# Kernel optimization log

Measured on AMD Instinct MI355X. Metric: run time of the kernel, lower is better.

Reference implementation:

```python
import jax, jax.numpy as jnp
import numpy as np

B, N, F = 8192, 48, 64      # batch, node_n, features
L = 11                      # stacked GraphConvolution blocks
EPS = 1e-5                  # BatchNorm1d eps


def setup_inputs() -> dict:
    key = jax.random.key(0)
    k0, k1, k2, k3, k4 = jax.random.split(key, 5)
    x = jax.random.normal(k0, (B, N, F), dtype=jnp.float32)
    # xavier-normal-ish GC weights, all layers are F->F (in==out)
    W = jax.random.normal(k1, (L, F, F), dtype=jnp.float32) * np.sqrt(2.0 / (F + F)).astype(np.float32)
    # att init: 0.01 + 0.99 * I  (learned node-mixing matrix)
    att = jnp.tile((0.01 + 0.99 * jnp.eye(N, dtype=jnp.float32))[None], (L, 1, 1))
    bias = 0.02 * jax.random.normal(k2, (L, F), dtype=jnp.float32)
    gamma = 1.0 + 0.1 * jax.random.normal(k3, (L, N * F), dtype=jnp.float32)
    beta = 0.1 * jax.random.normal(k4, (L, N * F), dtype=jnp.float32)
    return {"x": x, "W": W, "att": att, "bias": bias, "gamma": gamma, "beta": beta}


def _gcn_forward(x, W, att, bias, gamma, beta):
    def gc(h, i):
        # support = h @ W[i]; output = att[i] @ support + bias[i]
        support = jnp.einsum('bnf,fg->bng', h, W[i])
        return jnp.einsum('nm,bmg->bng', att[i], support) + bias[i]

    def bn(h, i):
        # BatchNorm1d over flattened (node_n * features), batch statistics
        b = h.shape[0]
        flat = h.reshape(b, -1)
        mu = jnp.mean(flat, axis=0)
        var = jnp.var(flat, axis=0)
        flat = (flat - mu) * jax.lax.rsqrt(var + EPS) * gamma[i] + beta[i]
        return flat.reshape(h.shape)

    def block(h, i):
        return jax.nn.sigmoid(bn(gc(h, i), i))  # dropout p=0 -> identity

    y1 = block(x, 0)
    y2 = block(y1, 1)
    y3 = block(y2, 2)
    y4 = block(y3, 3)
    y5 = block(y4, 4)
    y6 = block(y5, 5)
    y7 = block(y6 + y5, 6)
    y8 = block(y7 + y4, 7)
    y9 = block(y8 + y3, 8)
    y10 = block(y9 + y2, 9)
    y11 = block(y10 + y1, 10)  # in_features == out_features
    return y11 + x


def reference(x, W, att, bias, gamma, beta):
    return _gcn_forward(x, W, att, bias, gamma, beta)
```

## Files before the change

### kernel.cpp

```cpp
#include <hip/hip_runtime.h>

#define NBATCH 8192
#define NFEAT  3072
#define TOT    ((size_t)NBATCH * NFEAT)
#define ZBYTES (TOT * 2)
#define YBYTES (TOT)

typedef unsigned short u16;
typedef unsigned int   u32;
typedef unsigned char  u8;

typedef __attribute__((ext_vector_type(8))) short bf16x8;
typedef __attribute__((ext_vector_type(4))) float f32x4;

__device__ __forceinline__ float sigm(float u) {
  return 1.0f / (1.0f + __expf(-u));
}
__device__ __forceinline__ u16 f2b(float f) {
  const u32 u = __float_as_uint(f);
  return (u16)((u + 0x7FFFu + ((u >> 16) & 1u)) >> 16);
}
__device__ __forceinline__ float b2f(u16 h) {
  return __uint_as_float(((u32)h) << 16);
}
__device__ __forceinline__ u32 pack2(float a, float b) {
  return (u32)f2b(a) | ((u32)f2b(b) << 16);
}

template <int MODE>
__global__ __launch_bounds__(256, 2)
void gcn_layer(const void* in0v,
               const u8*  yres_in,
               u8*        yres_out,
               u16*       zout,
               const float* __restrict__ Wg,
               const float* __restrict__ Ag,
               const float* __restrict__ biasg,
               const float* __restrict__ gam0,
               const float* __restrict__ bet0,
               const float* __restrict__ sum0,
               const float* __restrict__ sq0,
               float* __restrict__ osum,
               float* __restrict__ osq)
{
  __shared__ __align__(16) char HlB[2][6144];
  __shared__ __align__(16) char STB[8192];

  const int t    = threadIdx.x;
  const int lane = t & 63;
  const int wv   = t >> 6;
  const int lr   = lane & 15;
  const int lk   = lane >> 4;

  bf16x8 Wf[2];
  #pragma unroll
  for (int ks = 0; ks < 2; ++ks)
    #pragma unroll
    for (int j = 0; j < 8; ++j) {
      const int k = ks * 32 + lk * 8 + j;
      Wf[ks][j] = (short)f2b(Wg[k * 64 + wv * 16 + lr]);
    }
  bf16x8 Af[3][2];
  #pragma unroll
  for (int nt = 0; nt < 3; ++nt)
    #pragma unroll
    for (int ks = 0; ks < 2; ++ks)
      #pragma unroll
      for (int j = 0; j < 8; ++j) {
        const int m = ks * 32 + lk * 8 + j;
        Af[nt][ks][j] = (m < 48) ? (short)f2b(Ag[(nt * 16 + lr) * 48 + m])
                                 : (short)0;
      }
  const float4 bi = *(const float4*)(biasg + wv * 16 + lk * 4);

  {
    const int row = t >> 2, ch = t & 3;
    const int off = (96 + ch * 8) ^ ((row & 7) << 4);
    *(uint2*)(STB + row * 128 + off) = make_uint2(0u, 0u);
  }

  const float invB = 1.0f / 8192.0f;
  float sc0[12], sh0[12];
  if (MODE >= 1) {
    #pragma unroll
    for (int q = 0; q < 3; ++q) {
      const int j = (t + 256 * q) * 4;
      #pragma unroll
      for (int c = 0; c < 4; ++c) {
        const float mu = sum0[j + c] * invB;
        const float va = fmaf(-mu, mu, sq0[j + c] * invB);
        const float s  = gam0[j + c] * rsqrtf(va + 1e-5f);
        sc0[q * 4 + c] = s;
        sh0[q * 4 + c] = fmaf(-mu, s, bet0[j + c]);
      }
    }
  }

  float ssum[12], ssq[12];
  #pragma unroll
  for (int i = 0; i < 12; ++i) { ssum[i] = 0.f; ssq[i] = 0.f; }

  const int stride = gridDim.x;

  float4  vcf[3], vnf[3];
  ushort4 vcb[3], vnb[3];
  uchar4  ucb[3], unb[3];
  {
    if (MODE == 0) {
      const float4* p0 = (const float4*)((const float*)in0v + (size_t)blockIdx.x * NFEAT);
      #pragma unroll
      for (int q = 0; q < 3; ++q) vcf[q] = p0[t + 256 * q];
    } else {
      const ushort4* p0 = (const ushort4*)((const u16*)in0v + (size_t)blockIdx.x * NFEAT);
      #pragma unroll
      for (int q = 0; q < 3; ++q) vcb[q] = p0[t + 256 * q];
      if (MODE == 2) {
        const uchar4* p1 = (const uchar4*)(yres_in + (size_t)blockIdx.x * NFEAT);
        #pragma unroll
        for (int q = 0; q < 3; ++q) ucb[q] = p1[t + 256 * q];
      }
    }
  }

  __syncthreads();

  int buf = 0;
  for (int b = blockIdx.x; b < NBATCH; b += stride, buf ^= 1) {
    #pragma unroll
    for (int q = 0; q < 3; ++q) {
      float4 v;
      if (MODE == 0) {
        v = vcf[q];
      } else {
        v = make_float4(b2f(vcb[q].x), b2f(vcb[q].y), b2f(vcb[q].z), b2f(vcb[q].w));
        v.x = sigm(fmaf(v.x, sc0[q * 4 + 0], sh0[q * 4 + 0]));
        v.y = sigm(fmaf(v.y, sc0[q * 4 + 1], sh0[q * 4 + 1]));
        v.z = sigm(fmaf(v.z, sc0[q * 4 + 2], sh0[q * 4 + 2]));
        v.w = sigm(fmaf(v.w, sc0[q * 4 + 3], sh0[q * 4 + 3]));
        if (MODE == 1) {
          uchar4 yq;
          yq.x = (u8)fmaf(v.x, 255.f, 0.5f);
          yq.y = (u8)fmaf(v.y, 255.f, 0.5f);
          yq.z = (u8)fmaf(v.z, 255.f, 0.5f);
          yq.w = (u8)fmaf(v.w, 255.f, 0.5f);
          *(uchar4*)(yres_out + (size_t)b * NFEAT + (size_t)(t + 256 * q) * 4) = yq;
        }
        if (MODE == 2) {
          v.x += (float)ucb[q].x * (1.f / 255.f);
          v.y += (float)ucb[q].y * (1.f / 255.f);
          v.z += (float)ucb[q].z * (1.f / 255.f);
          v.w += (float)ucb[q].w * (1.f / 255.f);
        }
      }
      const int j   = (t + 256 * q) * 4;
      const int row = j >> 6;
      const int cb  = (j & 63) * 2;
      *(uint2*)(HlB[buf] + row * 128 + (cb ^ ((row & 7) << 4))) =
          make_uint2(pack2(v.x, v.y), pack2(v.z, v.w));
    }

    {
      const int bn = (b + stride < NBATCH) ? (b + stride) : b;
      if (MODE == 0) {
        const float4* p0 = (const float4*)((const float*)in0v + (size_t)bn * NFEAT);
        #pragma unroll
        for (int q = 0; q < 3; ++q) vnf[q] = p0[t + 256 * q];
      } else {
        const ushort4* p0 = (const ushort4*)((const u16*)in0v + (size_t)bn * NFEAT);
        #pragma unroll
        for (int q = 0; q < 3; ++q) vnb[q] = p0[t + 256 * q];
        if (MODE == 2) {
          const uchar4* p1 = (const uchar4*)(yres_in + (size_t)bn * NFEAT);
          #pragma unroll
          for (int q = 0; q < 3; ++q) unb[q] = p1[t + 256 * q];
        }
      }
    }

    __syncthreads();

    #pragma unroll
    for (int mt = 0; mt < 3; ++mt) {
      f32x4 acc = {0.f, 0.f, 0.f, 0.f};
      #pragma unroll
      for (int ks = 0; ks < 2; ++ks) {
        const int row = mt * 16 + lr;
        const int off = (ks * 64 + lk * 16) ^ ((row & 7) << 4);
        const bf16x8 aF = *(const bf16x8*)(HlB[buf] + row * 128 + off);
        acc = __builtin_amdgcn_mfma_f32_16x16x32_bf16(aF, Wf[ks], acc, 0, 0, 0);
      }
      const int g   = wv * 16 + lr;
      const int off = (mt * 32 + lk * 8) ^ ((g & 7) << 4);
      *(uint2*)(STB + g * 128 + off) =
          make_uint2(pack2(acc[0], acc[1]), pack2(acc[2], acc[3]));
    }

    bf16x8 sF[2];
    {
      const int g = wv * 16 + lr;
      #pragma unroll
      for (int ks = 0; ks < 2; ++ks) {
        const int off = (ks * 64 + lk * 16) ^ ((g & 7) << 4);
        sF[ks] = *(const bf16x8*)(STB + g * 128 + off);
      }
    }
    u16* zp = zout + (size_t)b * NFEAT;
    #pragma unroll
    for (int nt = 0; nt < 3; ++nt) {
      f32x4 acc = {0.f, 0.f, 0.f, 0.f};
      acc = __builtin_amdgcn_mfma_f32_16x16x32_bf16(sF[0], Af[nt][0], acc, 0, 0, 0);
      acc = __builtin_amdgcn_mfma_f32_16x16x32_bf16(sF[1], Af[nt][1], acc, 0, 0, 0);
      const int n  = nt * 16 + lr;
      const int gb = wv * 16 + lk * 4;
      const float v0 = acc[0] + bi.x;
      const float v1 = acc[1] + bi.y;
      const float v2 = acc[2] + bi.z;
      const float v3 = acc[3] + bi.w;
      ushort4 zq;
      zq.x = f2b(v0); zq.y = f2b(v1); zq.z = f2b(v2); zq.w = f2b(v3);
      *(ushort4*)(zp + n * 64 + gb) = zq;
      const float vr[4] = {b2f(zq.x), b2f(zq.y), b2f(zq.z), b2f(zq.w)};
      #pragma unroll
      for (int c = 0; c < 4; ++c) {
        ssum[nt * 4 + c] += vr[c];
        ssq[nt * 4 + c]   = fmaf(vr[c], vr[c], ssq[nt * 4 + c]);
      }
    }

    #pragma unroll
    for (int q = 0; q < 3; ++q) {
      if (MODE == 0) vcf[q] = vnf[q];
      else           vcb[q] = vnb[q];
      if (MODE == 2) ucb[q] = unb[q];
    }
  }

  #pragma unroll
  for (int r = 0; r < 3; ++r) {
    #pragma unroll
    for (int c = 0; c < 4; ++c) {
      const int j = (r * 16 + lr) * 64 + wv * 16 + lk * 4 + c;
      atomicAdd(&osum[j], ssum[r * 4 + c]);
      atomicAdd(&osq[j],  ssq[r * 4 + c]);
    }
  }
}

__global__ __launch_bounds__(256)
void gcn_final(const u16* __restrict__ z,
               const float* __restrict__ xin,
               const float* __restrict__ gam,
               const float* __restrict__ bet,
               const float* __restrict__ sum,
               const float* __restrict__ sq,
               float* __restrict__ outp)
{
  const float invB = 1.0f / 8192.0f;
  const int total4 = (int)(TOT / 4);
  const int stride = gridDim.x * blockDim.x;
  for (int i4 = blockIdx.x * blockDim.x + threadIdx.x; i4 < total4; i4 += stride) {
    const int j = (i4 % 768) * 4;
    const ushort4 zq = ((const ushort4*)z)[i4];
    const float4  xv = ((const float4*)xin)[i4];
    const float zz[4] = {b2f(zq.x), b2f(zq.y), b2f(zq.z), b2f(zq.w)};
    const float xx[4] = {xv.x, xv.y, xv.z, xv.w};
    float o[4];
    #pragma unroll
    for (int c = 0; c < 4; ++c) {
      const float mu = sum[j + c] * invB;
      const float va = fmaf(-mu, mu, sq[j + c] * invB);
      const float s  = gam[j + c] * rsqrtf(va + 1e-5f);
      const float sh = fmaf(-mu, s, bet[j + c]);
      o[c] = sigm(fmaf(zz[c], s, sh)) + xx[c];
    }
    ((float4*)outp)[i4] = make_float4(o[0], o[1], o[2], o[3]);
  }
}

extern "C" void kernel_launch(void* const* d_in, const int* in_sizes, int n_in,
                              void* d_out, int out_size, void* d_ws, size_t ws_size,
                              hipStream_t stream)
{
  const float* x    = (const float*)d_in[0];
  const float* W    = (const float*)d_in[1];
  const float* att  = (const float*)d_in[2];
  const float* bias = (const float*)d_in[3];
  const float* gam  = (const float*)d_in[4];
  const float* bet  = (const float*)d_in[5];
  float* out = (float*)d_out;

  u8* y1 = (u8*)d_out;
  u8* y2 = y1 + TOT;
  u8* y3 = y2 + TOT;
  u8* y4 = y3 + TOT;

  const size_t statbytes = (size_t)2 * 11 * NFEAT * 4;
  const size_t need = ZBYTES + YBYTES + statbytes;
  if (ws_size < need) {
    hipMemcpyAsync(out, x, TOT * 4, hipMemcpyDeviceToDevice, stream);
    return;
  }

  char* wsb = (char*)d_ws;
  u16* chain = (u16*)wsb;
  u8*  y5    = (u8*)(wsb + ZBYTES);
  float* stats = (float*)(wsb + ZBYTES + YBYTES);
  hipMemsetAsync(stats, 0, statbytes, stream);

  auto sumP = [&](int l) { return stats + (size_t)l * NFEAT; };
  auto sqP  = [&](int l) { return stats + (size_t)(11 + l) * NFEAT; };

  const dim3 grd(512), blk(256);
  auto G = [&](int mode, const void* i0, const u8* yin, u8* yout, int k) {
    const int p = (k > 0) ? (k - 1) : 0;
    const float* Wk = W + (size_t)k * 4096;
    const float* Ak = att + (size_t)k * 2304;
    const float* bk = bias + (size_t)k * 64;
    const float* g0p = gam + (size_t)p * NFEAT;
    const float* b0p = bet + (size_t)p * NFEAT;
    if (mode == 0)
      gcn_layer<0><<<grd, blk, 0, stream>>>(i0, yin, yout, chain, Wk, Ak, bk,
          g0p, b0p, sumP(p), sqP(p), sumP(k), sqP(k));
    else if (mode == 1)
      gcn_layer<1><<<grd, blk, 0, stream>>>(i0, yin, yout, chain, Wk, Ak, bk,
          g0p, b0p, sumP(p), sqP(p), sumP(k), sqP(k));
    else
      gcn_layer<2><<<grd, blk, 0, stream>>>(i0, yin, yout, chain, Wk, Ak, bk,
          g0p, b0p, sumP(p), sqP(p), sumP(k), sqP(k));
  };

  G(0, x,     nullptr, y1, 0);
  G(1, chain, nullptr, y1, 1);
  G(1, chain, nullptr, y2, 2);
  G(1, chain, nullptr, y3, 3);
  G(1, chain, nullptr, y4, 4);
  G(1, chain, nullptr, y5, 5);
  G(2, chain, y5, nullptr, 6);
  G(2, chain, y4, nullptr, 7);
  G(2, chain, y3, nullptr, 8);
  G(2, chain, y2, nullptr, 9);
  G(2, chain, y1, nullptr, 10);
  gcn_final<<<dim3(2048), blk, 0, stream>>>(chain, x, gam + (size_t)10 * NFEAT,
                                            bet + (size_t)10 * NFEAT,
                                            sumP(10), sqP(10), out);
}
```

Measured before the change: 1.808 ms.

## Batch eight samples per stage with deep register prefetch and eight LDS buffers

The per-sample double-buffered loop becomes a two-stage schedule. Each stage issues global loads for 8 batch rows at once, converts all of them into 8 separate LDS tiles, then runs the two MFMA GEMMs over each tile. The second stage's loads are issued right after the first stage's tiles are staged, so more memory requests are in flight to hide HBM latency. The cost is much higher register pressure, with spill risk, and roughly 56KB of LDS per block. It also hardcodes the grid and an exact count of 16 samples per block.

```diff
diff --git a/kernel.cpp b/kernel.cpp
--- a/kernel.cpp
+++ b/kernel.cpp
@@ -5,6 +5,7 @@
 #define TOT    ((size_t)NBATCH * NFEAT)
 #define ZBYTES (TOT * 2)
 #define YBYTES (TOT)
+#define GRID   512
 
 typedef unsigned short u16;
 typedef unsigned int   u32;
@@ -43,7 +44,7 @@
                float* __restrict__ osum,
                float* __restrict__ osq)
 {
-  __shared__ __align__(16) char HlB[2][6144];
+  __shared__ __align__(16) char HlB[8][6144];
   __shared__ __align__(16) char STB[8192];
 
   const int t    = threadIdx.x;
@@ -100,139 +101,139 @@
   #pragma unroll
   for (int i = 0; i < 12; ++i) { ssum[i] = 0.f; ssq[i] = 0.f; }
 
-  const int stride = gridDim.x;
-
-  float4  vcf[3], vnf[3];
-  ushort4 vcb[3], vnb[3];
-  uchar4  ucb[3], unb[3];
-  {
-    if (MODE == 0) {
-      const float4* p0 = (const float4*)((const float*)in0v + (size_t)blockIdx.x * NFEAT);
-      #pragma unroll
-      for (int q = 0; q < 3; ++q) vcf[q] = p0[t + 256 * q];
-    } else {
-      const ushort4* p0 = (const ushort4*)((const u16*)in0v + (size_t)blockIdx.x * NFEAT);
-      #pragma unroll
-      for (int q = 0; q < 3; ++q) vcb[q] = p0[t + 256 * q];
-      if (MODE == 2) {
-        const uchar4* p1 = (const uchar4*)(yres_in + (size_t)blockIdx.x * NFEAT);
-        #pragma unroll
-        for (int q = 0; q < 3; ++q) ucb[q] = p1[t + 256 * q];
-      }
-    }
-  }
-
-  __syncthreads();
-
-  int buf = 0;
-  for (int b = blockIdx.x; b < NBATCH; b += stride, buf ^= 1) {
-    #pragma unroll
-    for (int q = 0; q < 3; ++q) {
-      float4 v;
+  float4  fst[8][3];
+  ushort4 vst[8][3];
+  uchar4  yst[8][3];
+  uchar4  yq [8][3];
+
+  auto issue = [&](int s) {
+    #pragma unroll
+    for (int e = 0; e < 8; ++e) {
+      const int b = blockIdx.x + (s * 8 + e) * GRID;
       if (MODE == 0) {
-        v = vcf[q];
+        const float4* p = (const float4*)((const float*)in0v + (size_t)b * NFEAT);
+        #pragma unroll
+        for (int q = 0; q < 3; ++q) fst[e][q] = p[t + 256 * q];
       } else {
-        v = make_float4(b2f(vcb[q].x), b2f(vcb[q].y), b2f(vcb[q].z), b2f(vcb[q].w));
-        v.x = sigm(fmaf(v.x, sc0[q * 4 + 0], sh0[q * 4 + 0]));
-        v.y = sigm(fmaf(v.y, sc0[q * 4 + 1], sh0[q * 4 + 1]));
-        v.z = sigm(fmaf(v.z, sc0[q * 4 + 2], sh0[q * 4 + 2]));
-        v.w = sigm(fmaf(v.w, sc0[q * 4 + 3], sh0[q * 4 + 3]));
-        if (MODE == 1) {
-          uchar4 yq;
-          yq.x = (u8)fmaf(v.x, 255.f, 0.5f);
-          yq.y = (u8)fmaf(v.y, 255.f, 0.5f);
-          yq.z = (u8)fmaf(v.z, 255.f, 0.5f);
-          yq.w = (u8)fmaf(v.w, 255.f, 0.5f);
-          *(uchar4*)(yres_out + (size_t)b * NFEAT + (size_t)(t + 256 * q) * 4) = yq;
-        }
+        const ushort4* p = (const ushort4*)((const u16*)in0v + (size_t)b * NFEAT);
+        #pragma unroll
+        for (int q = 0; q < 3; ++q) vst[e][q] = p[t + 256 * q];
         if (MODE == 2) {
-          v.x += (float)ucb[q].x * (1.f / 255.f);
-          v.y += (float)ucb[q].y * (1.f / 255.f);
-          v.z += (float)ucb[q].z * (1.f / 255.f);
-          v.w += (float)ucb[q].w * (1.f / 255.f);
-        }
-      }
-      const int j   = (t + 256 * q) * 4;
-      const int row = j >> 6;
-      const int cb  = (j & 63) * 2;
-      *(uint2*)(HlB[buf] + row * 128 + (cb ^ ((row & 7) << 4))) =
-          make_uint2(pack2(v.x, v.y), pack2(v.z, v.w));
-    }
-
-    {
-      const int bn = (b + stride < NBATCH) ? (b + stride) : b;
-      if (MODE == 0) {
-        const float4* p0 = (const float4*)((const float*)in0v + (size_t)bn * NFEAT);
-        #pragma unroll
-        for (int q = 0; q < 3; ++q) vnf[q] = p0[t + 256 * q];
-      } else {
-        const ushort4* p0 = (const ushort4*)((const u16*)in0v + (size_t)bn * NFEAT);
-        #pragma unroll
-        for (int q = 0; q < 3; ++q) vnb[q] = p0[t + 256 * q];
-        if (MODE == 2) {
-          const uchar4* p1 = (const uchar4*)(yres_in + (size_t)bn * NFEAT);
+          const uchar4* py = (const uchar4*)(yres_in + (size_t)b * NFEAT);
           #pragma unroll
-          for (int q = 0; q < 3; ++q) unb[q] = p1[t + 256 * q];
-        }
+          for (int q = 0; q < 3; ++q) yst[e][q] = py[t + 256 * q];
+        }
+      }
+    }
+  };
+
+  issue(0);
+
+  for (int s = 0; s < 2; ++s) {
+    #pragma unroll
+    for (int e = 0; e < 8; ++e) {
+      #pragma unroll
+      for (int q = 0; q < 3; ++q) {
+        float4 v;
+        if (MODE == 0) {
+          v = fst[e][q];
+        } else {
+          v = make_float4(b2f(vst[e][q].x), b2f(vst[e][q].y),
+                          b2f(vst[e][q].z), b2f(vst[e][q].w));
+          v.x = sigm(fmaf(v.x, sc0[q * 4 + 0], sh0[q * 4 + 0]));
+          v.y = sigm(fmaf(v.y, sc0[q * 4 + 1], sh0[q * 4 + 1]));
+          v.z = sigm(fmaf(v.z, sc0[q * 4 + 2], sh0[q * 4 + 2]));
+          v.w = sigm(fmaf(v.w, sc0[q * 4 + 3], sh0[q * 4 + 3]));
+          if (MODE == 1) {
+            yq[e][q].x = (u8)fmaf(v.x, 255.f, 0.5f);
+            yq[e][q].y = (u8)fmaf(v.y, 255.f, 0.5f);
+            yq[e][q].z = (u8)fmaf(v.z, 255.f, 0.5f);
+            yq[e][q].w = (u8)fmaf(v.w, 255.f, 0.5f);
+          }
+          if (MODE == 2) {
+            v.x += (float)yst[e][q].x * (1.f / 255.f);
+            v.y += (float)yst[e][q].y * (1.f / 255.f);
+            v.z += (float)yst[e][q].z * (1.f / 255.f);
+            v.w += (float)yst[e][q].w * (1.f / 255.f);
+          }
+        }
+        const int j   = (t + 256 * q) * 4;
+        const int row = j >> 6;
+        const int cb  = (j & 63) * 2;
+        *(uint2*)(HlB[e] + row * 128 + (cb ^ ((row & 7) << 4))) =
+            make_uint2(pack2(v.x, v.y), pack2(v.z, v.w));
       }
     }
 
     __syncthreads();
 
-    #pragma unroll
-    for (int mt = 0; mt < 3; ++mt) {
-      f32x4 acc = {0.f, 0.f, 0.f, 0.f};
-      #pragma unroll
-      for (int ks = 0; ks < 2; ++ks) {
-        const int row = mt * 16 + lr;
-        const int off = (ks * 64 + lk * 16) ^ ((row & 7) << 4);
-        const bf16x8 aF = *(const bf16x8*)(HlB[buf] + row * 128 + off);
-        acc = __builtin_amdgcn_mfma_f32_16x16x32_bf16(aF, Wf[ks], acc, 0, 0, 0);
-      }
-      const int g   = wv * 16 + lr;
-      const int off = (mt * 32 + lk * 8) ^ ((g & 7) << 4);
-      *(uint2*)(STB + g * 128 + off) =
-          make_uint2(pack2(acc[0], acc[1]), pack2(acc[2], acc[3]));
-    }
-
-    bf16x8 sF[2];
-    {
-      const int g = wv * 16 + lr;
-      #pragma unroll
-      for (int ks = 0; ks < 2; ++ks) {
-        const int off = (ks * 64 + lk * 16) ^ ((g & 7) << 4);
-        sF[ks] = *(const bf16x8*)(STB + g * 128 + off);
-      }
-    }
-    u16* zp = zout + (size_t)b * NFEAT;
-    #pragma unroll
-    for (int nt = 0; nt < 3; ++nt) {
-      f32x4 acc = {0.f, 0.f, 0.f, 0.f};
-      acc = __builtin_amdgcn_mfma_f32_16x16x32_bf16(sF[0], Af[nt][0], acc, 0, 0, 0);
-      acc = __builtin_amdgcn_mfma_f32_16x16x32_bf16(sF[1], Af[nt][1], acc, 0, 0, 0);
-      const int n  = nt * 16 + lr;
-      const int gb = wv * 16 + lk * 4;
-      const float v0 = acc[0] + bi.x;
-      const float v1 = acc[1] + bi.y;
-      const float v2 = acc[2] + bi.z;
-      const float v3 = acc[3] + bi.w;
-      ushort4 zq;
-      zq.x = f2b(v0); zq.y = f2b(v1); zq.z = f2b(v2); zq.w = f2b(v3);
-      *(ushort4*)(zp + n * 64 + gb) = zq;
-      const float vr[4] = {b2f(zq.x), b2f(zq.y), b2f(zq.z), b2f(zq.w)};
-      #pragma unroll
-      for (int c = 0; c < 4; ++c) {
-        ssum[nt * 4 + c] += vr[c];
-        ssq[nt * 4 + c]   = fmaf(vr[c], vr[c], ssq[nt * 4 + c]);
-      }
-    }
-
-    #pragma unroll
-    for (int q = 0; q < 3; ++q) {
-      if (MODE == 0) vcf[q] = vnf[q];
-      else           vcb[q] = vnb[q];
-      if (MODE == 2) ucb[q] = unb[q];
-    }
+    if (s == 0) issue(1);
+
+    if (MODE == 1) {
+      #pragma unroll
+      for (int e = 0; e < 8; ++e) {
+        const int b = blockIdx.x + (s * 8 + e) * GRID;
+        #pragma unroll
+        for (int q = 0; q < 3; ++q)
+          *(uchar4*)(yres_out + (size_t)b * NFEAT + (size_t)(t + 256 * q) * 4)
+              = yq[e][q];
+      }
+    }
+
+    #pragma unroll
+    for (int e = 0; e < 8; ++e) {
+      const int b = blockIdx.x + (s * 8 + e) * GRID;
+
+      #pragma unroll
+      for (int mt = 0; mt < 3; ++mt) {
+        f32x4 acc = {0.f, 0.f, 0.f, 0.f};
+        #pragma unroll
+        for (int ks = 0; ks < 2; ++ks) {
+          const int row = mt * 16 + lr;
+          const int off = (ks * 64 + lk * 16) ^ ((row & 7) << 4);
+          const bf16x8 aF = *(const bf16x8*)(HlB[e] + row * 128 + off);
+          acc = __builtin_amdgcn_mfma_f32_16x16x32_bf16(aF, Wf[ks], acc, 0, 0, 0);
+        }
+        const int g   = wv * 16 + lr;
+        const int off = (mt * 32 + lk * 8) ^ ((g & 7) << 4);
+        *(uint2*)(STB + g * 128 + off) =
+            make_uint2(pack2(acc[0], acc[1]), pack2(acc[2], acc[3]));
+      }
+
+      bf16x8 sF[2];
+      {
+        const int g = wv * 16 + lr;
+        #pragma unroll
+        for (int ks = 0; ks < 2; ++ks) {
+          const int off = (ks * 64 + lk * 16) ^ ((g & 7) << 4);
+          sF[ks] = *(const bf16x8*)(STB + g * 128 + off);
+        }
+      }
+      u16* zp = zout + (size_t)b * NFEAT;
+      #pragma unroll
+      for (int nt = 0; nt < 3; ++nt) {
+        f32x4 acc = {0.f, 0.f, 0.f, 0.f};
+        acc = __builtin_amdgcn_mfma_f32_16x16x32_bf16(sF[0], Af[nt][0], acc, 0, 0, 0);
+        acc = __builtin_amdgcn_mfma_f32_16x16x32_bf16(sF[1], Af[nt][1], acc, 0, 0, 0);
+        const int n  = nt * 16 + lr;
+        const int gb = wv * 16 + lk * 4;
+        const float v0 = acc[0] + bi.x;
+        const float v1 = acc[1] + bi.y;
+        const float v2 = acc[2] + bi.z;
+        const float v3 = acc[3] + bi.w;
+        ushort4 zq4;
+        zq4.x = f2b(v0); zq4.y = f2b(v1); zq4.z = f2b(v2); zq4.w = f2b(v3);
+        *(ushort4*)(zp + n * 64 + gb) = zq4;
+        const float vr[4] = {b2f(zq4.x), b2f(zq4.y), b2f(zq4.z), b2f(zq4.w)};
+        #pragma unroll
+        for (int c = 0; c < 4; ++c) {
+          ssum[nt * 4 + c] += vr[c];
+          ssq[nt * 4 + c]   = fmaf(vr[c], vr[c], ssq[nt * 4 + c]);
+        }
+      }
+    }
+
+    __syncthreads();
   }
 
   #pragma unroll
@@ -310,7 +311,7 @@
   auto sumP = [&](int l) { return stats + (size_t)l * NFEAT; };
   auto sqP  = [&](int l) { return stats + (size_t)(11 + l) * NFEAT; };
 
-  const dim3 grd(512), blk(256);
+  const dim3 grd(GRID), blk(256);
   auto G = [&](int mode, const void* i0, const u8* yin, u8* yout, int k) {
     const int p = (k > 0) ? (k - 1) : 0;
     const float* Wk = W + (size_t)k * 4096;
```

Result: slower. 1.864 ms (+3.1%).
